# Optimization experiments

Hardware: AMD Instinct MI355X
Metric: run time of the kernel (lower is better)

## Reference

```python
import jax, jax.numpy as jnp
import numpy as np

H = 1024      # hidden_dim
NH = 16       # num_heads
HD = H // NH  # head_dim
FF = 4 * H
EPS = 1e-5

def _ln(x, g, b):
    m = jnp.mean(x, axis=-1, keepdims=True)
    v = jnp.var(x, axis=-1, keepdims=True)
    return (x - m) * jax.lax.rsqrt(v + EPS) * g + b

def setup_inputs() -> dict:
    key = jax.random.key(0)
    ks = jax.random.split(key, 12)
    s = 1.0 / np.sqrt(H)
    inp = {
        'x': jax.random.normal(ks[0], (2, 2048, H), dtype=jnp.float32),
        'Wq': jax.random.normal(ks[1], (H, H), dtype=jnp.float32) * s,
        'bq': jnp.zeros((H,), dtype=jnp.float32),
        'Wk': jax.random.normal(ks[2], (H, H), dtype=jnp.float32) * s,
        'bk': jnp.zeros((H,), dtype=jnp.float32),
        'Wv': jax.random.normal(ks[3], (H, H), dtype=jnp.float32) * s,
        'bv': jnp.zeros((H,), dtype=jnp.float32),
        'Wo': jax.random.normal(ks[4], (H, H), dtype=jnp.float32) * s,
        'bo': jnp.zeros((H,), dtype=jnp.float32),
        'g1': jnp.ones((H,), dtype=jnp.float32),
        'b1': jnp.zeros((H,), dtype=jnp.float32),
        'W1': jax.random.normal(ks[5], (H, FF), dtype=jnp.float32) * s,
        'bf1': jnp.zeros((FF,), dtype=jnp.float32),
        'W2': jax.random.normal(ks[6], (FF, H), dtype=jnp.float32) * (1.0 / np.sqrt(FF)),
        'bf2': jnp.zeros((H,), dtype=jnp.float32),
        'g2': jnp.ones((H,), dtype=jnp.float32),
        'b2': jnp.zeros((H,), dtype=jnp.float32),
    }
    return inp

def reference(x, Wq, bq, Wk, bk, Wv, bv, Wo, bo, g1, b1, W1, bf1, W2, bf2, g2, b2):
    B, S, _ = x.shape
    residual = x
    xn = _ln(x, g1, b1)
    # [B,S,H] -> [B,NH,S,HD]
    def split_heads(t):
        return t.reshape(B, S, NH, HD).transpose(0, 2, 1, 3)
    q = split_heads(xn @ Wq + bq)
    k = split_heads(xn @ Wk + bk)
    v = split_heads(xn @ Wv + bv)
    scores = jnp.einsum('bhqd,bhkd->bhqk', q, k) / np.sqrt(HD).astype(np.float32)
    attn = jax.nn.softmax(scores, axis=-1)
    ctx = jnp.einsum('bhqk,bhkd->bhqd', attn, v)
    ctx = ctx.transpose(0, 2, 1, 3).reshape(B, S, H)
    out = ctx @ Wo + bo + residual
    residual = out
    on = _ln(out, g2, b2)
    out = jax.nn.relu(on @ W1 + bf1) @ W2 + bf2 + residual
    return out
```

## Files before the change

### kernel.cpp

```cpp
#include <hip/hip_runtime.h>
#include <hip/hip_bf16.h>

constexpr int HDIM = 1024;
constexpr int NHEAD = 16;
constexpr int FFDIM = 4096;
constexpr int SEQLEN = 2048;
constexpr int NTOK = 4096;

typedef __bf16 bf16x8 __attribute__((ext_vector_type(8)));
typedef float f32x4 __attribute__((ext_vector_type(4)));
typedef short s16x4 __attribute__((ext_vector_type(4)));

union U16x8 {
    s16x4 h[2];
    bf16x8 v;
    int4 raw;
    short s[8];
};

__device__ __forceinline__ short f2bf(float f) {
    __hip_bfloat16 h = __float2bfloat16(f);
    return *reinterpret_cast<short*>(&h);
}

__device__ __forceinline__ void gload16(const void* gsrc, void* lds) {
    __builtin_amdgcn_global_load_lds(
        (const __attribute__((address_space(1))) unsigned int*)gsrc,
        (__attribute__((address_space(3))) unsigned int*)lds, 16, 0, 0);
}


constexpr float QSCALE = 0.18033688011112042f;

__global__ __launch_bounds__(256)
void wconv_all(const float* __restrict__ Wq, const float* __restrict__ Wk,
               const float* __restrict__ Wv, const float* __restrict__ Wo,
               const float* __restrict__ W1, const float* __restrict__ W2,
               short* __restrict__ qkvT, short* __restrict__ WoT,
               short* __restrict__ W1T, short* __restrict__ W2T) {
    int i = blockIdx.x;
    const float* W;
    short* WT;
    int K, N, bx, by;
    if (i < 2048) {
        const int w = i >> 9;
        i &= 511;
        K = HDIM; N = HDIM; bx = i & 3; by = i >> 2;
        W = w == 0 ? Wq : w == 1 ? Wk : w == 2 ? Wv : Wo;
        WT = w == 3 ? WoT : qkvT + (size_t)w * HDIM * HDIM;
    } else if (i < 4096) {
        i -= 2048;
        K = HDIM; N = FFDIM; bx = i & 15; by = i >> 4;
        W = W1; WT = W1T;
    } else {
        i -= 4096;
        K = FFDIM; N = HDIM; bx = i & 3; by = i >> 2;
        W = W2; WT = W2T;
    }
    const int n = bx * 256 + threadIdx.x;
    const int g = by >> 2, fc = by & 3;
    const int k0 = g * 32 + fc * 4;
    s16x4 lo, hi;
#pragma unroll
    for (int j = 0; j < 4; ++j) lo[j] = f2bf(W[(size_t)(k0 + j) * N + n]);
#pragma unroll
    for (int j = 0; j < 4; ++j) hi[j] = f2bf(W[(size_t)(k0 + 16 + j) * N + n]);
    short* dst = WT + (size_t)n * K + by * 8;
    *(s16x4*)dst = lo;
    *(s16x4*)(dst + 4) = hi;
}

__global__ __launch_bounds__(256)
void ln_bf16(const float* __restrict__ x, const float* __restrict__ g,
             const float* __restrict__ b, short* __restrict__ out) {
    const int row = blockIdx.x, t = threadIdx.x;
    const float* xr = x + (size_t)row * HDIM;
    float4 v = *(const float4*)&xr[t * 4];
    float s = v.x + v.y + v.z + v.w;
    float ss = v.x * v.x + v.y * v.y + v.z * v.z + v.w * v.w;
#pragma unroll
    for (int o = 32; o > 0; o >>= 1) {
        s += __shfl_down(s, o);
        ss += __shfl_down(ss, o);
    }
    __shared__ float red[8];
    const int wv = t >> 6, ln = t & 63;
    if (ln == 0) { red[wv] = s; red[4 + wv] = ss; }
    __syncthreads();
    s = red[0] + red[1] + red[2] + red[3];
    ss = red[4] + red[5] + red[6] + red[7];
    const float mean = s * (1.0f / HDIM);
    const float var = ss * (1.0f / HDIM) - mean * mean;
    const float rstd = rsqrtf(var + 1e-5f);
    float4 gv = *(const float4*)&g[t * 4];
    float4 bv = *(const float4*)&b[t * 4];
    s16x4 o4;
    o4[0] = f2bf((v.x - mean) * rstd * gv.x + bv.x);
    o4[1] = f2bf((v.y - mean) * rstd * gv.y + bv.y);
    o4[2] = f2bf((v.z - mean) * rstd * gv.z + bv.z);
    o4[3] = f2bf((v.w - mean) * rstd * gv.w + bv.w);
    const int kk = (t * 4) & 31;
    const int dst = ((t * 4) & ~31) + ((kk & 15) >> 2) * 8 + (kk >> 4) * 4;
    *(s16x4*)&out[(size_t)row * HDIM + dst] = o4;
}

template <int BM, int BN, int MODE>
__global__ __launch_bounds__(256, 3)
void gemm_bf16(const short* __restrict__ A, const short* __restrict__ BT,
               const float* __restrict__ bias, const float* __restrict__ resid,
               void* __restrict__ outp, int M, int N, int K,
               const float* __restrict__ bias2, const float* __restrict__ bias3,
               void* __restrict__ out3) {
    constexpr int MI = BM / 32, NJ = BN / 32;
    constexpr int NSEG = (BM + BN) / 16;
    __shared__ short LdsF[2 * (BM + BN) * 32];
    const int tid = threadIdx.x;
    const int lane = tid & 63, wave = tid >> 6;
    const int wm = wave >> 1, wn = wave & 1;
    const int l15 = lane & 15, lg = lane >> 4;
    const int lsw = lg ^ ((l15 >> 1) & 3);
    const int m0 = blockIdx.x * BM, n0 = blockIdx.y * BN;
    const int nk = K >> 5;
    const int sr = lane >> 2;
    const int sc8 = (((lane & 3) ^ ((sr >> 1) & 3))) * 8;

    auto stage = [&](int buf, int kt) {
#pragma unroll
        for (int p = 0; p < NSEG / 4; ++p) {
            const int s = wave + p * 4;
            const short* src = (s < BM / 16)
                ? A + (size_t)(m0 + s * 16 + sr) * K + kt * 32 + sc8
                : BT + (size_t)(n0 + (s - BM / 16) * 16 + sr) * K + kt * 32 + sc8;
            const int off = __builtin_amdgcn_readfirstlane(buf * (BM + BN) * 64 + s * 1024);
            gload16(src, (char*)LdsF + off);
        }
    };

    f32x4 acc[MI][NJ] = {};
    stage(0, 0);
    for (int kt = 0; kt < nk; ++kt) {
        const int buf = kt & 1;
        __syncthreads();
        if (kt + 1 < nk) stage(buf ^ 1, kt + 1);
        bf16x8 af[MI], bfr[NJ];
#pragma unroll
        for (int i = 0; i < MI; ++i)
            af[i] = *(const bf16x8*)&LdsF[buf * (BM + BN) * 32 +
                                          (wm * (BM / 2) + i * 16 + l15) * 32 + lsw * 8];
#pragma unroll
        for (int j = 0; j < NJ; ++j)
            bfr[j] = *(const bf16x8*)&LdsF[buf * (BM + BN) * 32 +
                                           (BM + wn * (BN / 2) + j * 16 + l15) * 32 + lsw * 8];
#pragma unroll
        for (int i = 0; i < MI; ++i)
#pragma unroll
            for (int j = 0; j < NJ; ++j)
                acc[i][j] = __builtin_amdgcn_mfma_f32_16x16x32_bf16(af[i], bfr[j], acc[i][j], 0, 0, 0);
    }

    const int rbase = m0 + wm * (BM / 2);
    const int cbase = n0 + wn * (BN / 2);
    if constexpr (MODE == 0) {
#pragma unroll
        for (int i = 0; i < MI; ++i)
#pragma unroll
            for (int j = 0; j < NJ; ++j) {
                const int c = cbase + j * 16 + l15;
                const float bv = bias[c];
#pragma unroll
                for (int ii = 0; ii < 4; ++ii) {
                    const int r = rbase + i * 16 + lg * 4 + ii;
                    const size_t idx = (size_t)r * N + c;
                    ((float*)outp)[idx] = acc[i][j][ii] + bv + resid[idx];
                }
            }
    } else if constexpr (MODE == 1) {
#pragma unroll
        for (int i = 0; i < MI; ++i)
#pragma unroll
            for (int j = 0; j < NJ; ++j) {
                const int c = cbase + j * 16 + l15;
                const float bv = bias[c];
                const int cp = (c & ~31) | ((l15 >> 2) * 8 + (j & 1) * 4 + (l15 & 3));
#pragma unroll
                for (int ii = 0; ii < 4; ++ii) {
                    const int r = rbase + i * 16 + lg * 4 + ii;
                    float v = acc[i][j][ii] + bv;
                    v = v > 0.0f ? v : 0.0f;
                    ((short*)outp)[(size_t)r * N + cp] = f2bf(v);
                }
            }
    } else {
        const int which = n0 >> 10;
        if (which < 2) {
            const float* bb = which == 0 ? bias : bias2;
            const float qs = which == 0 ? QSCALE : 1.0f;
            short* QKp = (short*)outp;
#pragma unroll
            for (int i = 0; i < MI; ++i)
#pragma unroll
                for (int j = 0; j < NJ; ++j) {
                    const int c = cbase + j * 16 + l15;
                    const float bv = bb[c & 1023];
                    const int cp = (c & ~31) | ((l15 >> 2) * 8 + (j & 1) * 4 + (l15 & 3));
#pragma unroll
                    for (int ii = 0; ii < 4; ++ii) {
                        const int r = rbase + i * 16 + lg * 4 + ii;
                        QKp[(size_t)r * 2048 + cp] = f2bf((acc[i][j][ii] + bv) * qs);
                    }
                }
        } else {
            short* VTp = (short*)out3;
#pragma unroll
            for (int j = 0; j < NJ; ++j) {
                const int c = cbase + j * 16 + l15;
                const int cc = c - 2048;
                const int hh = cc >> 6, dd = cc & 63;
                const float bv = bias3[cc];
#pragma unroll
                for (int i = 0; i < MI; ++i) {
                    const int r0 = rbase + i * 16 + lg * 4;
                    const int bb_ = r0 >> 11;
                    const int s0 = r0 & (SEQLEN - 1);
                    const int sbase = (s0 & ~31) + lg * 8 + (i & 1) * 4;
                    s16x4 v4;
#pragma unroll
                    for (int ii = 0; ii < 4; ++ii) v4[ii] = f2bf(acc[i][j][ii] + bv);
                    *(s16x4*)&VTp[(((size_t)(bb_ * NHEAD + hh)) * 64 + dd) * SEQLEN + sbase] = v4;
                }
            }
        }
    }
}

__global__ __launch_bounds__(256, 3)
void attn_fwd(const short* __restrict__ QK, const short* __restrict__ VT,
              short* __restrict__ ctx) {
    __shared__ short KlF[2 * 4096];
    __shared__ short VlF[2 * 4096];
    const int tid = threadIdx.x, lane = tid & 63, wave = tid >> 6;
    const int l15 = lane & 15, lg = lane >> 4;
    const int lsw = lg ^ ((l15 >> 1) & 3);
    const int qt = blockIdx.x, bh = blockIdx.y;
    const int b = bh >> 4, h = bh & 15;
    const size_t tokbase = (size_t)b * SEQLEN;
    const short* Kbase = QK + 1024 + h * 64;
    const short* Vbase = VT + (size_t)bh * 64 * SEQLEN;
    const int sr = lane >> 2;
    const int sc8 = (((lane & 3) ^ ((sr >> 1) & 3))) * 8;

    auto stage = [&](int buf, int kt) {
#pragma unroll
        for (int p = 0; p < 2; ++p) {
            const int seg = wave + p * 4;
            const int ks = seg >> 2, rb = (seg & 3) * 16;
            const int off = __builtin_amdgcn_readfirstlane(buf * 8192 + seg * 1024);
            gload16(Kbase + (tokbase + kt * 64 + rb + sr) * 2048 + ks * 32 + sc8,
                    (char*)KlF + off);
            gload16(Vbase + (size_t)(rb + sr) * SEQLEN + kt * 64 + ks * 32 + sc8,
                    (char*)VlF + off);
        }
    };

    const short* qp = QK + (tokbase + qt * 64 + wave * 16 + l15) * 2048 + h * 64;
    bf16x8 qf[2];
    qf[0] = *(const bf16x8*)(qp + lg * 8);
    qf[1] = *(const bf16x8*)(qp + 32 + lg * 8);

    f32x4 o[4] = {};
    float Mi = -INFINITY, Li = 0.0f;
    stage(0, 0);
    for (int kt = 0; kt < SEQLEN / 64; ++kt) {
        const int buf = kt & 1;
        __syncthreads();
        if (kt + 1 < SEQLEN / 64) stage(buf ^ 1, kt + 1);

        f32x4 sc[4];
        __builtin_amdgcn_s_setprio(1);
#pragma unroll
        for (int j = 0; j < 4; ++j) {
            bf16x8 kf0 = *(const bf16x8*)&KlF[buf * 4096 + (j * 16 + l15) * 32 + lsw * 8];
            bf16x8 kf1 = *(const bf16x8*)&KlF[buf * 4096 + 2048 + (j * 16 + l15) * 32 + lsw * 8];
            f32x4 z = {};
            z = __builtin_amdgcn_mfma_f32_16x16x32_bf16(kf0, qf[0], z, 0, 0, 0);
            sc[j] = __builtin_amdgcn_mfma_f32_16x16x32_bf16(kf1, qf[1], z, 0, 0, 0);
        }
        __builtin_amdgcn_s_setprio(0);

        float pmax = -INFINITY;
#pragma unroll
        for (int j = 0; j < 4; ++j)
            pmax = fmaxf(pmax, fmaxf(fmaxf(sc[j][0], sc[j][1]), fmaxf(sc[j][2], sc[j][3])));
        pmax = fmaxf(pmax, __shfl_xor(pmax, 16));
        pmax = fmaxf(pmax, __shfl_xor(pmax, 32));
        if (__any(pmax > Mi + 8.0f)) {
            const float newM = fmaxf(Mi, pmax);
            const float fac = exp2f(Mi - newM);
            Li *= fac;
#pragma unroll
            for (int fd = 0; fd < 4; ++fd) o[fd] *= fac;
            Mi = newM;
        }
        float pr[4][4];
        float sum = 0.0f;
#pragma unroll
        for (int j = 0; j < 4; ++j)
#pragma unroll
            for (int ii = 0; ii < 4; ++ii) {
                const float p = exp2f(sc[j][ii] - Mi);
                pr[j][ii] = p;
                sum += p;
            }
        sum += __shfl_xor(sum, 16);
        sum += __shfl_xor(sum, 32);
        Li += sum;

        U16x8 u0, u1;
#pragma unroll
        for (int ii = 0; ii < 4; ++ii) {
            u0.s[ii] = f2bf(pr[0][ii]);
            u0.s[4 + ii] = f2bf(pr[1][ii]);
            u1.s[ii] = f2bf(pr[2][ii]);
            u1.s[4 + ii] = f2bf(pr[3][ii]);
        }
        __builtin_amdgcn_s_setprio(1);
#pragma unroll
        for (int ks = 0; ks < 2; ++ks) {
            const bf16x8 pf = ks == 0 ? u0.v : u1.v;
#pragma unroll
            for (int fd = 0; fd < 4; ++fd) {
                bf16x8 vf = *(const bf16x8*)&VlF[buf * 4096 + ks * 2048 + (fd * 16 + l15) * 32 + lsw * 8];
                o[fd] = __builtin_amdgcn_mfma_f32_16x16x32_bf16(vf, pf, o[fd], 0, 0, 0);
            }
        }
        __builtin_amdgcn_s_setprio(0);
    }

    const float rl = 1.0f / Li;
    const int qrow = qt * 64 + wave * 16 + l15;
    short* crow = ctx + (tokbase + qrow) * HDIM + h * 64;
#pragma unroll
    for (int fd = 0; fd < 4; ++fd) {
        s16x4 v4;
#pragma unroll
        for (int ii = 0; ii < 4; ++ii) v4[ii] = f2bf(o[fd][ii] * rl);
        *(s16x4*)(crow + (fd >> 1) * 32 + lg * 8 + (fd & 1) * 4) = v4;
    }
}

extern "C" void kernel_launch(void* const* d_in, const int* in_sizes, int n_in,
                              void* d_out, int out_size, void* d_ws, size_t ws_size,
                              hipStream_t stream) {
    const float* x  = (const float*)d_in[0];
    const float* Wq = (const float*)d_in[1];
    const float* bq = (const float*)d_in[2];
    const float* Wk = (const float*)d_in[3];
    const float* bk = (const float*)d_in[4];
    const float* Wv = (const float*)d_in[5];
    const float* bv = (const float*)d_in[6];
    const float* Wo = (const float*)d_in[7];
    const float* bo = (const float*)d_in[8];
    const float* g1 = (const float*)d_in[9];
    const float* b1 = (const float*)d_in[10];
    const float* W1 = (const float*)d_in[11];
    const float* bf1 = (const float*)d_in[12];
    const float* W2 = (const float*)d_in[13];
    const float* bf2 = (const float*)d_in[14];
    const float* g2 = (const float*)d_in[15];
    const float* b2 = (const float*)d_in[16];

    char* ws = (char*)d_ws;
    const size_t MB = 1024 * 1024;
    short* qkvT = (short*)(ws + 0 * MB);
    short* WoT  = (short*)(ws + 6 * MB);
    short* W1T  = (short*)(ws + 8 * MB);
    short* W2T  = (short*)(ws + 16 * MB);
    short* xn   = (short*)(ws + 24 * MB);
    short* QKb  = (short*)(ws + 32 * MB);
    short* VTb  = (short*)(ws + 48 * MB);
    short* ctx  = (short*)(ws + 56 * MB);
    float* out1 = (float*)(ws + 64 * MB);
    short* h1   = (short*)(ws + 32 * MB);

    wconv_all<<<6144, 256, 0, stream>>>(Wq, Wk, Wv, Wo, W1, W2, qkvT, WoT, W1T, W2T);

    ln_bf16<<<NTOK, 256, 0, stream>>>(x, g1, b1, xn);

    gemm_bf16<128, 128, 2><<<dim3(NTOK / 128, 3072 / 128), 256, 0, stream>>>(
        xn, qkvT, bq, nullptr, QKb, NTOK, 3072, HDIM, bk, bv, VTb);

    attn_fwd<<<dim3(SEQLEN / 64, 32), 256, 0, stream>>>(QKb, VTb, ctx);

    gemm_bf16<128, 64, 0><<<dim3(NTOK / 128, HDIM / 64), 256, 0, stream>>>(
        ctx, WoT, bo, x, out1, NTOK, HDIM, HDIM, nullptr, nullptr, nullptr);

    ln_bf16<<<NTOK, 256, 0, stream>>>(out1, g2, b2, xn);

    gemm_bf16<128, 128, 1><<<dim3(NTOK / 128, FFDIM / 128), 256, 0, stream>>>(
        xn, W1T, bf1, nullptr, h1, NTOK, FFDIM, HDIM, nullptr, nullptr, nullptr);

    gemm_bf16<128, 64, 0><<<dim3(NTOK / 128, HDIM / 64), 256, 0, stream>>>(
        h1, W2T, bf2, out1, (float*)d_out, NTOK, HDIM, FFDIM, nullptr, nullptr, nullptr);
}
```

Baseline: 247.5 us.

## Compute softmax row sums via MFMA with ones vector and raise attention occupancy

The attention kernel drops the per-element VALU sum and the cross-lane shuffles for the softmax denominator. It accumulates the denominator with an extra MFMA against a ones vector, so the sum comes from the same bf16-rounded probabilities used for P·V. The bf16 conversion becomes a simple round-half-up bit trick without NaN handling, the max reduction is rebalanced into a shallower tree, and launch bounds move from 3 to 4 waves per SIMD. The higher occupancy target may force register spilling, and the row sum now carries bf16 rounding.

```diff
diff --git a/kernel.cpp b/kernel.cpp
--- a/kernel.cpp
+++ b/kernel.cpp
@@ -19,8 +19,9 @@
 };
 
 __device__ __forceinline__ short f2bf(float f) {
-    __hip_bfloat16 h = __float2bfloat16(f);
-    return *reinterpret_cast<short*>(&h);
+    union { float f; unsigned u; } c;
+    c.f = f;
+    return (short)((c.u + 0x8000u) >> 16);
 }
 
 __device__ __forceinline__ void gload16(const void* gsrc, void* lds) {
@@ -233,7 +234,7 @@
     }
 }
 
-__global__ __launch_bounds__(256, 3)
+__global__ __launch_bounds__(256, 4)
 void attn_fwd(const short* __restrict__ QK, const short* __restrict__ VT,
               short* __restrict__ ctx) {
     __shared__ short KlF[2 * 4096];
@@ -267,8 +268,14 @@
     qf[0] = *(const bf16x8*)(qp + lg * 8);
     qf[1] = *(const bf16x8*)(qp + 32 + lg * 8);
 
+    U16x8 uo;
+#pragma unroll
+    for (int j = 0; j < 8; ++j) uo.s[j] = 0x3F80;
+    const bf16x8 onesv = uo.v;
+
     f32x4 o[4] = {};
-    float Mi = -INFINITY, Li = 0.0f;
+    f32x4 Lacc = {};
+    float Mi = -INFINITY;
     stage(0, 0);
     for (int kt = 0; kt < SEQLEN / 64; ++kt) {
         const int buf = kt & 1;
@@ -287,46 +294,37 @@
         }
         __builtin_amdgcn_s_setprio(0);
 
-        float pmax = -INFINITY;
-#pragma unroll
-        for (int j = 0; j < 4; ++j)
-            pmax = fmaxf(pmax, fmaxf(fmaxf(sc[j][0], sc[j][1]), fmaxf(sc[j][2], sc[j][3])));
+        const float a0 = fmaxf(fmaxf(sc[0][0], sc[0][1]), sc[0][2]);
+        const float a1 = fmaxf(fmaxf(sc[0][3], sc[1][0]), sc[1][1]);
+        const float a2 = fmaxf(fmaxf(sc[1][2], sc[1][3]), sc[2][0]);
+        const float a3 = fmaxf(fmaxf(sc[2][1], sc[2][2]), sc[2][3]);
+        const float a4 = fmaxf(fmaxf(sc[3][0], sc[3][1]), sc[3][2]);
+        const float b0 = fmaxf(fmaxf(a0, a1), sc[3][3]);
+        const float b1 = fmaxf(fmaxf(a2, a3), a4);
+        float pmax = fmaxf(b0, b1);
         pmax = fmaxf(pmax, __shfl_xor(pmax, 16));
         pmax = fmaxf(pmax, __shfl_xor(pmax, 32));
         if (__any(pmax > Mi + 8.0f)) {
             const float newM = fmaxf(Mi, pmax);
             const float fac = exp2f(Mi - newM);
-            Li *= fac;
+            Lacc *= fac;
 #pragma unroll
             for (int fd = 0; fd < 4; ++fd) o[fd] *= fac;
             Mi = newM;
         }
-        float pr[4][4];
-        float sum = 0.0f;
-#pragma unroll
-        for (int j = 0; j < 4; ++j)
-#pragma unroll
-            for (int ii = 0; ii < 4; ++ii) {
-                const float p = exp2f(sc[j][ii] - Mi);
-                pr[j][ii] = p;
-                sum += p;
-            }
-        sum += __shfl_xor(sum, 16);
-        sum += __shfl_xor(sum, 32);
-        Li += sum;
-
         U16x8 u0, u1;
 #pragma unroll
         for (int ii = 0; ii < 4; ++ii) {
-            u0.s[ii] = f2bf(pr[0][ii]);
-            u0.s[4 + ii] = f2bf(pr[1][ii]);
-            u1.s[ii] = f2bf(pr[2][ii]);
-            u1.s[4 + ii] = f2bf(pr[3][ii]);
+            u0.s[ii]     = f2bf(exp2f(sc[0][ii] - Mi));
+            u0.s[4 + ii] = f2bf(exp2f(sc[1][ii] - Mi));
+            u1.s[ii]     = f2bf(exp2f(sc[2][ii] - Mi));
+            u1.s[4 + ii] = f2bf(exp2f(sc[3][ii] - Mi));
         }
         __builtin_amdgcn_s_setprio(1);
 #pragma unroll
         for (int ks = 0; ks < 2; ++ks) {
             const bf16x8 pf = ks == 0 ? u0.v : u1.v;
+            Lacc = __builtin_amdgcn_mfma_f32_16x16x32_bf16(onesv, pf, Lacc, 0, 0, 0);
 #pragma unroll
             for (int fd = 0; fd < 4; ++fd) {
                 bf16x8 vf = *(const bf16x8*)&VlF[buf * 4096 + ks * 2048 + (fd * 16 + l15) * 32 + lsw * 8];
@@ -336,7 +334,7 @@
         __builtin_amdgcn_s_setprio(0);
     }
 
-    const float rl = 1.0f / Li;
+    const float rl = 1.0f / Lacc[0];
     const int qrow = qt * 64 + wave * 16 + l15;
     short* crow = ctx + (tokbase + qrow) * HDIM + h * 64;
 #pragma unroll
```

New measurement: 246.1 us. About the same (-0.6%).
